# Kernel tuning notes

Measured on AMD Instinct MI355X. Metric: run time of the kernel, lower is better.

## Reference

```python
import jax, jax.numpy as jnp
import numpy as np

N, E, H, L, IN, OUT = 50000, 800000, 64, 14, 128, 112
MSG_EPS = 1e-7   # GENConv message epsilon
LN_EPS = 1e-5    # torch.nn.LayerNorm default eps


def setup_inputs() -> dict:
    key = jax.random.key(0)
    ks = jax.random.split(key, 8)
    s = 0.05
    x = jax.random.normal(ks[0], (N, IN), jnp.float32)
    edge_index = jax.random.randint(ks[1], (2, E), 0, N, dtype=jnp.int64)
    enc_W = jax.random.normal(ks[2], (IN, H), jnp.float32) * s
    enc_b = jnp.zeros((H,), jnp.float32)
    ln_g = jnp.ones((L, H), jnp.float32)
    ln_b = jnp.zeros((L, H), jnp.float32)
    mlp_W = jax.random.normal(ks[3], (L, H, H), jnp.float32) * s
    mlp_b = jnp.zeros((L, H), jnp.float32)
    pred_W = jax.random.normal(ks[4], (H, OUT), jnp.float32) * s
    pred_b = jnp.zeros((OUT,), jnp.float32)
    return dict(x=x, edge_index=edge_index, enc_W=enc_W, enc_b=enc_b,
                ln_g=ln_g, ln_b=ln_b, mlp_W=mlp_W, mlp_b=mlp_b,
                pred_W=pred_W, pred_b=pred_b)


def _layernorm(h, g, b):
    mu = jnp.mean(h, axis=-1, keepdims=True)
    var = jnp.mean(jnp.square(h - mu), axis=-1, keepdims=True)  # biased, as torch
    return (h - mu) * jax.lax.rsqrt(var + LN_EPS) * g + b


def _genconv(h, src, dst, W, b):
    # GENConv: msg = relu(x_src) + eps; softmax aggregation (t=1) over dst; out = Linear(x + agg)
    msg = jax.nn.relu(h[src]) + MSG_EPS                    # [E, H]
    mmax = jax.ops.segment_max(msg, dst, num_segments=N)   # [N, H]
    mmax = jnp.where(jnp.isfinite(mmax), mmax, 0.0)         # empty segments
    ex = jnp.exp(msg - mmax[dst])                           # [E, H]
    denom = jax.ops.segment_sum(ex, dst, num_segments=N)    # [N, H]
    num = jax.ops.segment_sum(msg * ex, dst, num_segments=N)
    agg = num / jnp.maximum(denom, 1e-16)                   # 0 for isolated nodes
    return (h + agg) @ W + b


def reference(x, edge_index, enc_W, enc_b, ln_g, ln_b, mlp_W, mlp_b, pred_W, pred_b):
    src, dst = edge_index[0], edge_index[1]
    h = x @ enc_W + enc_b                       # node feature encoder
    h = _genconv(h, src, dst, mlp_W[0], mlp_b[0])  # first GCN (no pre-norm in res+)

    def body(h, params):
        g, bl, W, b = params
        h2 = jax.nn.relu(_layernorm(h, g, bl))  # dropout is identity (eval)
        h = _genconv(h2, src, dst, W, b) + h    # residual
        return h, None

    h, _ = jax.lax.scan(body, h, (ln_g[:L - 1], ln_b[:L - 1], mlp_W[1:], mlp_b[1:]))
    return h @ pred_W + pred_b
```

## Files before the change

kernel.cpp:

```cpp
#include <hip/hip_runtime.h>
#include <hip/hip_bf16.h>

#define NN 50000
#define EE 800000
#define HD 64
#define LL 14
#define IND 128
#define OUTD 112
#define LN2 0.69314718056f

typedef __attribute__((ext_vector_type(8))) short short8;
typedef __attribute__((ext_vector_type(4))) float float4_;
typedef __attribute__((ext_vector_type(4))) unsigned short ushort4_;

__device__ __forceinline__ short bf16_hi(float x) {
    return (short)(__float_as_uint(x) >> 16);
}
__device__ __forceinline__ float bf16_f(short s) {
    return __uint_as_float(((unsigned)(unsigned short)s) << 16);
}
__device__ __forceinline__ unsigned short f2b_rne(float x) {
    unsigned u = __float_as_uint(x);
    u += 0x7fffu + ((u >> 16) & 1u);
    return (unsigned short)(u >> 16);
}

__device__ __forceinline__ void split8(const float* p, short8& hi, short8& lo) {
    float4_ a = *(const float4_*)p;
    float4_ b = *(const float4_*)(p + 4);
    float v[8] = {a[0], a[1], a[2], a[3], b[0], b[1], b[2], b[3]};
    #pragma unroll
    for (int j = 0; j < 8; ++j) {
        short h = bf16_hi(v[j]);
        hi[j] = h;
        lo[j] = bf16_hi(v[j] - bf16_f(h));
    }
}

__device__ __forceinline__ void load_b(const float* __restrict__ W, int ldw,
                                       int colbase, int krow, short8& hi, short8& lo) {
    #pragma unroll
    for (int j = 0; j < 8; ++j) {
        float wv = W[(krow + j) * ldw + colbase];
        short h = bf16_hi(wv);
        hi[j] = h;
        lo[j] = bf16_hi(wv - bf16_f(h));
    }
}

__device__ __forceinline__ float4_ mm3(short8 ah, short8 al, short8 bh, short8 bl,
                                       float4_ acc) {
    acc = __builtin_amdgcn_mfma_f32_16x16x32_bf16(ah, bh, acc, 0, 0, 0);
    acc = __builtin_amdgcn_mfma_f32_16x16x32_bf16(al, bh, acc, 0, 0, 0);
    acc = __builtin_amdgcn_mfma_f32_16x16x32_bf16(ah, bl, acc, 0, 0, 0);
    return acc;
}

#define ACCQ(q, sv, nv) { \
    float p0_ = __uint_as_float((q).x << 16); \
    float p1_ = __uint_as_float((q).x & 0xffff0000u); \
    float p2_ = __uint_as_float((q).y << 16); \
    float p3_ = __uint_as_float((q).y & 0xffff0000u); \
    sv[0] += p0_; sv[1] += p1_; sv[2] += p2_; sv[3] += p3_; \
    nv[0] = fmaf(p0_, __log2f(p0_), nv[0]); \
    nv[1] = fmaf(p1_, __log2f(p1_), nv[1]); \
    nv[2] = fmaf(p2_, __log2f(p2_), nv[2]); \
    nv[3] = fmaf(p3_, __log2f(p3_), nv[3]); }


__global__ void k_hist(const int* __restrict__ ei, int* __restrict__ cnt,
                       int* __restrict__ rank) {
    int e = blockIdx.x * blockDim.x + threadIdx.x;
    if (e < EE) rank[e] = atomicAdd(&cnt[ei[EE + e]], 1);
}

__global__ __launch_bounds__(1024) void k_scan1(const int* __restrict__ deg,
                                                int* __restrict__ excl,
                                                int* __restrict__ bsum) {
    __shared__ int ws[16];
    int tid = threadIdx.x, lane = tid & 63, w = tid >> 6;
    int gid = blockIdx.x * 1024 + tid;
    int v = (gid < NN) ? deg[gid] : 0;
    int x = v;
    #pragma unroll
    for (int d = 1; d < 64; d <<= 1) {
        int y = __shfl_up(x, d);
        if (lane >= d) x += y;
    }
    if (lane == 63) ws[w] = x;
    __syncthreads();
    if (tid == 0) {
        int acc = 0;
        for (int i = 0; i < 16; i++) { int t = ws[i]; ws[i] = acc; acc += t; }
        bsum[blockIdx.x] = acc;
    }
    __syncthreads();
    if (gid < NN) excl[gid] = x - v + ws[w];
}

__global__ void k_scan2(const int* __restrict__ bsum, int* __restrict__ boff, int nb) {
    int lane = threadIdx.x & 63;
    int v = (lane < nb) ? bsum[lane] : 0;
    int x = v;
    #pragma unroll
    for (int d = 1; d < 64; d <<= 1) {
        int y = __shfl_up(x, d);
        if (lane >= d) x += y;
    }
    if (lane < nb) boff[lane] = x - v;
}

__global__ __launch_bounds__(1024) void k_scan3(int* __restrict__ rp,
                                                const int* __restrict__ boff) {
    int gid = blockIdx.x * 1024 + threadIdx.x;
    if (gid < NN) rp[gid] += boff[blockIdx.x];
    if (gid == 0) rp[NN] = EE;
}

__global__ void k_scatter(const int* __restrict__ ei, const int* __restrict__ rp,
                          const int* __restrict__ rank, int* __restrict__ csrc) {
    int e = blockIdx.x * blockDim.x + threadIdx.x;
    if (e < EE) {
        int d = ei[EE + e];
        csrc[rp[d] + rank[e]] = ei[e];
    }
}


__global__ __launch_bounds__(256) void k_dhist(const int* __restrict__ deg,
                                               int* __restrict__ bhist) {
    __shared__ int lh[64];
    int tid = threadIdx.x;
    if (tid < 64) lh[tid] = 0;
    __syncthreads();
    int n = blockIdx.x * 256 + tid;
    if (n < NN) atomicAdd(&lh[63 - min(deg[n], 63)], 1);
    __syncthreads();
    if (tid < 64 && lh[tid]) atomicAdd(&bhist[tid], lh[tid]);
}

__global__ void k_dscan(const int* __restrict__ bhist, int* __restrict__ gboff) {
    int lane = threadIdx.x & 63;
    int v = bhist[lane];
    int x = v;
    #pragma unroll
    for (int d = 1; d < 64; d <<= 1) {
        int y = __shfl_up(x, d);
        if (lane >= d) x += y;
    }
    gboff[lane] = x - v;
}

__global__ __launch_bounds__(256) void k_dscatter(const int* __restrict__ deg,
                                                  const int* __restrict__ rp,
                                                  int* __restrict__ gboff,
                                                  int4* __restrict__ nd) {
    __shared__ int lh[64], lbase[64];
    int tid = threadIdx.x;
    if (tid < 64) lh[tid] = 0;
    __syncthreads();
    int n = blockIdx.x * 256 + tid;
    int b = 0, lr = 0;
    if (n < NN) {
        b = 63 - min(deg[n], 63);
        lr = atomicAdd(&lh[b], 1);
    }
    __syncthreads();
    if (tid < 64) lbase[tid] = lh[tid] ? atomicAdd(&gboff[tid], lh[tid]) : 0;
    __syncthreads();
    if (n < NN) {
        int pos = lbase[b] + lr;
        nd[pos] = make_int4(n, rp[n], rp[n + 1] - rp[n], 0);
    }
}


__global__ __launch_bounds__(256) void k_enc(const float* __restrict__ x,
                                             const float* __restrict__ W,
                                             const float* __restrict__ b,
                                             float* __restrict__ h,
                                             unsigned short* __restrict__ P0,
                                             unsigned short* __restrict__ P1) {
    __shared__ float X[16 * 132];
    int tid = threadIdx.x, lane = tid & 63, w = tid >> 6;
    int nb = blockIdx.x * 16;
    int nq = lane >> 4, nr = lane & 15;
    int colbase = w * 16 + nr;

    if (blockIdx.x == 0 && tid < HD) {
        P0[(size_t)NN * HD + tid] = 0x3f80;
        P1[(size_t)NN * HD + tid] = 0x3f80;
    }

    {
        const float* src = x + (size_t)nb * IND + tid * 8;
        float4_ a = *(const float4_*)src;
        float4_ c = *(const float4_*)(src + 4);
        int m = tid >> 4, k8 = 8 * (tid & 15);
        *(float4_*)&X[m * 132 + k8] = a;
        *(float4_*)&X[m * 132 + k8 + 4] = c;
    }
    __syncthreads();

    float4_ acc = {};
    #pragma unroll
    for (int t = 0; t < 4; ++t) {
        short8 ah, al, bh, bl;
        split8(&X[nr * 132 + t * 32 + nq * 8], ah, al);
        load_b(W, HD, colbase, t * 32 + nq * 8, bh, bl);
        acc = mm3(ah, al, bh, bl, acc);
    }

    float bias = b[colbase];
    #pragma unroll
    for (int r = 0; r < 4; ++r) {
        int node = nb + nq * 4 + r;
        float y = acc[r] + bias;
        h[node * HD + colbase] = y;
        float msg = fminf(fmaxf(y, 0.f) + 1e-7f, 50.f);
        P0[node * HD + colbase] = f2b_rne(__expf(msg));
    }
}

__device__ __forceinline__ void gtail(const unsigned* __restrict__ Pb,
                                      const int* __restrict__ csrc,
                                      int beg, int deg, int g, int co, int lane,
                                      float4_& sv, float4_& nv, int& waste) {
    for (int chunk = 64; chunk < deg; chunk += 64) {
        int my = (chunk + lane < deg) ? csrc[beg + chunk + lane] : NN;
        int cnt = min(64, deg - chunk);
        int nb4 = (cnt + 3) >> 2;
        waste += nb4 * 4 - cnt;
        for (int k = 0; k < nb4; ++k) {
            int e = __shfl(my, k * 4 + g);
            uint2 q = *(const uint2*)(Pb + (((unsigned)e) << 5) + co);
            ACCQ(q, sv, nv);
        }
    }
}

__device__ __forceinline__ void finish_node(float4_ sv, float4_ nv, int waste,
                                            int pnode, int row, int g, int ci,
                                            const float* __restrict__ selfh,
                                            uint2 selfq, float* __restrict__ T) {
    float t0 = sv[0], t1 = sv[1], t2 = sv[2], t3 = sv[3];
    float u0 = nv[0], u1 = nv[1], u2 = nv[2], u3 = nv[3];
    #pragma unroll
    for (int d = 16; d < 64; d <<= 1) {
        t0 += __shfl_xor(t0, d); t1 += __shfl_xor(t1, d);
        t2 += __shfl_xor(t2, d); t3 += __shfl_xor(t3, d);
        u0 += __shfl_xor(u0, d); u1 += __shfl_xor(u1, d);
        u2 += __shfl_xor(u2, d); u3 += __shfl_xor(u3, d);
    }
    if (g == 0) {
        float wf = (float)waste;
        float a0 = LN2 * u0 / fmaxf(t0 - wf, 1e-16f);
        float a1 = LN2 * u1 / fmaxf(t1 - wf, 1e-16f);
        float a2 = LN2 * u2 / fmaxf(t2 - wf, 1e-16f);
        float a3 = LN2 * u3 / fmaxf(t3 - wf, 1e-16f);
        float4_ xv;
        if (selfh) {
            float4_ sf = *(const float4_*)&selfh[(size_t)pnode * HD + ci * 4];
            xv[0] = sf[0] + a0; xv[1] = sf[1] + a1;
            xv[2] = sf[2] + a2; xv[3] = sf[3] + a3;
        } else {
            unsigned d0 = selfq.x, d1 = selfq.y;
            xv[0] = LN2 * __log2f(__uint_as_float(d0 << 16)) - 1e-7f + a0;
            xv[1] = LN2 * __log2f(__uint_as_float(d0 & 0xffff0000u)) - 1e-7f + a1;
            xv[2] = LN2 * __log2f(__uint_as_float(d1 << 16)) - 1e-7f + a2;
            xv[3] = LN2 * __log2f(__uint_as_float(d1 & 0xffff0000u)) - 1e-7f + a3;
        }
        *(float4_*)&T[row * 68 + ci * 4] = xv;
    }
}

__global__ __launch_bounds__(256, 4) void k_layer(const unsigned short* __restrict__ Pin,
                                                  const float* __restrict__ selfh,
                                                  const float* __restrict__ hres,
                                                  float* __restrict__ hout,
                                                  unsigned short* __restrict__ Pout,
                                                  const int4* __restrict__ nd,
                                                  const int* __restrict__ csrc,
                                                  const float* __restrict__ W,
                                                  const float* __restrict__ b,
                                                  const float* __restrict__ gnext,
                                                  const float* __restrict__ bnext) {
    __shared__ float T[16 * 68];
    __shared__ int PN[16];
    int tid = threadIdx.x, lane = tid & 63, w = tid >> 6;
    int nb = blockIdx.x * 16;
    int nq = lane >> 4, nr = lane & 15;
    int colbase = w * 16 + nr;

    if (tid < 16) PN[tid] = nd[nb + tid].x;

    short8 Bhi[2], Blo[2];
    #pragma unroll
    for (int t = 0; t < 2; ++t)
        load_b(W, HD, colbase, t * 32 + nq * 8, Bhi[t], Blo[t]);

    int g = lane >> 4;
    int ci = lane & 15;
    int co = ci << 1;
    const unsigned* Pb = (const unsigned*)Pin;

    int4 dsc0 = nd[nb + w * 4 + 0];
    int4 dsc1 = nd[nb + w * 4 + 1];
    int4 dsc2 = nd[nb + w * 4 + 2];
    int4 dsc3 = nd[nb + w * 4 + 3];
    int p0n = dsc0.x, r0 = dsc0.y, dA = dsc0.z;
    int p1n = dsc1.x, r1 = dsc1.y, dB = dsc1.z;
    int p2n = dsc2.x, r2 = dsc2.y, dC = dsc2.z;
    int p3n = dsc3.x, r3 = dsc3.y, dD = dsc3.z;

    int myA = (lane < dA) ? csrc[r0 + lane] : NN;
    int myB = (lane < dB) ? csrc[r1 + lane] : NN;
    int myC = (lane < dC) ? csrc[r2 + lane] : NN;
    int myD = (lane < dD) ? csrc[r3 + lane] : NN;

    uint2 sq0 = {0, 0}, sq1 = {0, 0}, sq2 = {0, 0}, sq3 = {0, 0};
    if (!selfh) {
        sq0 = *(const uint2*)(Pb + (((unsigned)p0n) << 5) + co);
        sq1 = *(const uint2*)(Pb + (((unsigned)p1n) << 5) + co);
        sq2 = *(const uint2*)(Pb + (((unsigned)p2n) << 5) + co);
        sq3 = *(const uint2*)(Pb + (((unsigned)p3n) << 5) + co);
    }

    int cA = min(dA, 64), cB = min(dB, 64), cC = min(dC, 64), cD = min(dD, 64);
    int nk = (max(max(cA, cB), max(cC, cD)) + 3) >> 2;
    int wA = nk * 4 - cA, wB = nk * 4 - cB, wC = nk * 4 - cC, wD = nk * 4 - cD;

    float4_ sA = {}, nA = {}, sB = {}, nB = {}, sC = {}, nC = {}, sD = {}, nD = {};

    #pragma unroll 2
    for (int k = 0; k < nk; ++k) {
        int sidx = k * 4 + g;
        int e0 = __shfl(myA, sidx);
        int e1 = __shfl(myB, sidx);
        int e2 = __shfl(myC, sidx);
        int e3 = __shfl(myD, sidx);
        uint2 q0 = *(const uint2*)(Pb + (((unsigned)e0) << 5) + co);
        uint2 q1 = *(const uint2*)(Pb + (((unsigned)e1) << 5) + co);
        uint2 q2 = *(const uint2*)(Pb + (((unsigned)e2) << 5) + co);
        uint2 q3 = *(const uint2*)(Pb + (((unsigned)e3) << 5) + co);
        ACCQ(q0, sA, nA);
        ACCQ(q1, sB, nB);
        ACCQ(q2, sC, nC);
        ACCQ(q3, sD, nD);
    }
    if (dA > 64) gtail(Pb, csrc, r0, dA, g, co, lane, sA, nA, wA);
    if (dB > 64) gtail(Pb, csrc, r1, dB, g, co, lane, sB, nB, wB);
    if (dC > 64) gtail(Pb, csrc, r2, dC, g, co, lane, sC, nC, wC);
    if (dD > 64) gtail(Pb, csrc, r3, dD, g, co, lane, sD, nD, wD);

    finish_node(sA, nA, wA, p0n, w * 4 + 0, g, ci, selfh, sq0, T);
    finish_node(sB, nB, wB, p1n, w * 4 + 1, g, ci, selfh, sq1, T);
    finish_node(sC, nC, wC, p2n, w * 4 + 2, g, ci, selfh, sq2, T);
    finish_node(sD, nD, wD, p3n, w * 4 + 3, g, ci, selfh, sq3, T);
    __syncthreads();

    short8 Ahi[2], Alo[2];
    #pragma unroll
    for (int t = 0; t < 2; ++t)
        split8(&T[nr * 68 + t * 32 + nq * 8], Ahi[t], Alo[t]);
    __syncthreads();

    float4_ acc = {};
    #pragma unroll
    for (int t = 0; t < 2; ++t)
        acc = mm3(Ahi[t], Alo[t], Bhi[t], Blo[t], acc);

    float bias = b[colbase];
    #pragma unroll
    for (int r = 0; r < 4; ++r) {
        int m = nq * 4 + r;
        int pn = PN[m];
        float v = acc[r] + bias;
        if (hres) v += hres[pn * HD + colbase];
        hout[pn * HD + colbase] = v;
        T[m * 68 + colbase] = v;
    }
    if (!Pout) return;
    __syncthreads();

    int m = tid >> 4, c4 = (tid & 15) * 4;
    float4_ vv = *(const float4_*)&T[m * 68 + c4];
    float ps_ = (vv[0] + vv[1]) + (vv[2] + vv[3]);
    float pq_ = (vv[0] * vv[0] + vv[1] * vv[1]) + (vv[2] * vv[2] + vv[3] * vv[3]);
    #pragma unroll
    for (int d = 8; d; d >>= 1) {
        ps_ += __shfl_xor(ps_, d);
        pq_ += __shfl_xor(pq_, d);
    }
    float mu = ps_ * (1.f / 64.f);
    float var = pq_ * (1.f / 64.f) - mu * mu;
    float inv = rsqrtf(fmaxf(var, 0.f) + 1e-5f);
    float4_ g4 = *(const float4_*)&gnext[c4];
    float4_ b4 = *(const float4_*)&bnext[c4];
    ushort4_ po;
    #pragma unroll
    for (int j = 0; j < 4; ++j) {
        float y = fmaxf((vv[j] - mu) * inv * g4[j] + b4[j], 0.f);
        float msg = fminf(y + 1e-7f, 50.f);
        po[j] = f2b_rne(__expf(msg));
    }
    *(ushort4_*)&Pout[(size_t)PN[m] * HD + c4] = po;
}


__global__ __launch_bounds__(256) void k_pred(const float* __restrict__ h,
                                              const float* __restrict__ W,
                                              const float* __restrict__ b,
                                              float* __restrict__ out) {
    __shared__ float T[16 * 68];
    int tid = threadIdx.x, lane = tid & 63, w = tid >> 6;
    int nb = blockIdx.x * 16;
    int nq = lane >> 4, nr = lane & 15;

    {
        const float* src = h + (size_t)nb * HD + tid * 4;
        float4_ a = *(const float4_*)src;
        int m = tid >> 4, k4 = 4 * (tid & 15);
        *(float4_*)&T[m * 68 + k4] = a;
    }
    __syncthreads();

    short8 Ahi[2], Alo[2];
    #pragma unroll
    for (int t = 0; t < 2; ++t)
        split8(&T[nr * 68 + t * 32 + nq * 8], Ahi[t], Alo[t]);

    for (int tt = w; tt < 7; tt += 4) {
        int colbase = tt * 16 + nr;
        float4_ acc = {};
        #pragma unroll
        for (int t = 0; t < 2; ++t) {
            short8 bh, bl;
            load_b(W, OUTD, colbase, t * 32 + nq * 8, bh, bl);
            acc = mm3(Ahi[t], Alo[t], bh, bl, acc);
        }
        float bias = b[colbase];
        #pragma unroll
        for (int r = 0; r < 4; ++r) {
            int node = nb + nq * 4 + r;
            out[node * OUTD + colbase] = acc[r] + bias;
        }
    }
}


extern "C" void kernel_launch(void* const* d_in, const int* in_sizes, int n_in,
                              void* d_out, int out_size, void* d_ws, size_t ws_size,
                              hipStream_t stream) {
    const float* x    = (const float*)d_in[0];
    const int*   ei   = (const int*)d_in[1];
    const float* encW = (const float*)d_in[2];
    const float* encb = (const float*)d_in[3];
    const float* lng  = (const float*)d_in[4];
    const float* lnb  = (const float*)d_in[5];
    const float* mlpW = (const float*)d_in[6];
    const float* mlpb = (const float*)d_in[7];
    const float* pW   = (const float*)d_in[8];
    const float* pb   = (const float*)d_in[9];
    float* out = (float*)d_out;

    int4* nd = (int4*)d_ws;
    float* hA  = (float*)(nd + NN);
    float* hB  = hA + (size_t)NN * HD;
    unsigned short* PA = (unsigned short*)(hB + (size_t)NN * HD);
    unsigned short* PB = PA + (size_t)(NN + 1) * HD;
    int* rp    = (int*)(PB + (size_t)(NN + 1) * HD);
    int* cnt   = rp + (NN + 1);
    int* csrc  = cnt + NN;
    int* rank  = csrc + EE;
    int* bsum  = rank + EE;
    int* boff  = bsum + 64;
    int* bhist = boff + 64;
    int* gboff = bhist + 64;

    hipMemsetAsync(cnt, 0, NN * sizeof(int), stream);
    hipMemsetAsync(bhist, 0, 64 * sizeof(int), stream);
    k_hist<<<(EE + 255) / 256, 256, 0, stream>>>(ei, cnt, rank);
    const int NB = (NN + 1023) / 1024;
    k_scan1<<<NB, 1024, 0, stream>>>(cnt, rp, bsum);
    k_scan2<<<1, 64, 0, stream>>>(bsum, boff, NB);
    k_scan3<<<NB, 1024, 0, stream>>>(rp, boff);
    k_scatter<<<(EE + 255) / 256, 256, 0, stream>>>(ei, rp, rank, csrc);

    const int NDB = (NN + 255) / 256;
    k_dhist<<<NDB, 256, 0, stream>>>(cnt, bhist);
    k_dscan<<<1, 64, 0, stream>>>(bhist, gboff);
    k_dscatter<<<NDB, 256, 0, stream>>>(cnt, rp, gboff, nd);

    k_enc<<<NN / 16, 256, 0, stream>>>(x, encW, encb, hA, PA, PB);

    k_layer<<<NN / 16, 256, 0, stream>>>(PA, hA, nullptr, hB, PB, nd, csrc,
                                         mlpW, mlpb, lng, lnb);

    float* hres = hB;
    float* hdst = hA;
    unsigned short* pc = PB;
    unsigned short* pn = PA;
    for (int l = 1; l < LL; ++l) {
        bool last = (l == LL - 1);
        k_layer<<<NN / 16, 256, 0, stream>>>(pc, nullptr, hres, hdst,
                                             last ? nullptr : pn,
                                             nd, csrc,
                                             mlpW + (size_t)l * HD * HD,
                                             mlpb + (size_t)l * HD,
                                             last ? nullptr : lng + (size_t)l * HD,
                                             last ? nullptr : lnb + (size_t)l * HD);
        float* t = hres; hres = hdst; hdst = t;
        unsigned short* u = pc; pc = pn; pn = u;
    }

    k_pred<<<NN / 16, 256, 0, stream>>>(hres, pW, pb, out);
}
```

Before: 646.8 us.

## Gather 8 bf16 features per lane with 16-byte loads, processing nodes in pairs

The neighbor gather in the layer kernel now has each lane load a uint4 (8 bf16 values) instead of a uint2 (4 values). Eight edges are processed per wave step instead of four, and the cross-lane reduction gets one extra shuffle stage. The four destination nodes per wave are handled as two sequential pairs, which limits the growth in accumulator registers. The wider loads are meant to cut gather instruction count and raise bytes per request, but per-node padding waste grows with the 8-edge granularity, and only two rows are gathered concurrently instead of four, which lowers memory-level parallelism.

```diff
diff --git a/kernel.cpp b/kernel.cpp
--- a/kernel.cpp
+++ b/kernel.cpp
@@ -56,16 +56,25 @@
     return acc;
 }
 
-#define ACCQ(q, sv, nv) { \
+#define ACCQ8(q, sv, nv) { \
     float p0_ = __uint_as_float((q).x << 16); \
     float p1_ = __uint_as_float((q).x & 0xffff0000u); \
     float p2_ = __uint_as_float((q).y << 16); \
     float p3_ = __uint_as_float((q).y & 0xffff0000u); \
+    float p4_ = __uint_as_float((q).z << 16); \
+    float p5_ = __uint_as_float((q).z & 0xffff0000u); \
+    float p6_ = __uint_as_float((q).w << 16); \
+    float p7_ = __uint_as_float((q).w & 0xffff0000u); \
     sv[0] += p0_; sv[1] += p1_; sv[2] += p2_; sv[3] += p3_; \
+    sv[4] += p4_; sv[5] += p5_; sv[6] += p6_; sv[7] += p7_; \
     nv[0] = fmaf(p0_, __log2f(p0_), nv[0]); \
     nv[1] = fmaf(p1_, __log2f(p1_), nv[1]); \
     nv[2] = fmaf(p2_, __log2f(p2_), nv[2]); \
-    nv[3] = fmaf(p3_, __log2f(p3_), nv[3]); }
+    nv[3] = fmaf(p3_, __log2f(p3_), nv[3]); \
+    nv[4] = fmaf(p4_, __log2f(p4_), nv[4]); \
+    nv[5] = fmaf(p5_, __log2f(p5_), nv[5]); \
+    nv[6] = fmaf(p6_, __log2f(p6_), nv[6]); \
+    nv[7] = fmaf(p7_, __log2f(p7_), nv[7]); }
 
 
 __global__ void k_hist(const int* __restrict__ ei, int* __restrict__ cnt,
@@ -222,55 +231,54 @@
     }
 }
 
-__device__ __forceinline__ void gtail(const unsigned* __restrict__ Pb,
-                                      const int* __restrict__ csrc,
-                                      int beg, int deg, int g, int co, int lane,
-                                      float4_& sv, float4_& nv, int& waste) {
+__device__ __forceinline__ void gtail8(const unsigned* __restrict__ Pb,
+                                       const int* __restrict__ csrc,
+                                       int beg, int deg, int og, int co4, int lane,
+                                       float* s, float* n, int& waste) {
     for (int chunk = 64; chunk < deg; chunk += 64) {
+        int cnt = min(64, deg - chunk);
         int my = (chunk + lane < deg) ? csrc[beg + chunk + lane] : NN;
-        int cnt = min(64, deg - chunk);
-        int nb4 = (cnt + 3) >> 2;
-        waste += nb4 * 4 - cnt;
-        for (int k = 0; k < nb4; ++k) {
-            int e = __shfl(my, k * 4 + g);
-            uint2 q = *(const uint2*)(Pb + (((unsigned)e) << 5) + co);
-            ACCQ(q, sv, nv);
-        }
-    }
-}
-
-__device__ __forceinline__ void finish_node(float4_ sv, float4_ nv, int waste,
-                                            int pnode, int row, int g, int ci,
-                                            const float* __restrict__ selfh,
-                                            uint2 selfq, float* __restrict__ T) {
-    float t0 = sv[0], t1 = sv[1], t2 = sv[2], t3 = sv[3];
-    float u0 = nv[0], u1 = nv[1], u2 = nv[2], u3 = nv[3];
-    #pragma unroll
-    for (int d = 16; d < 64; d <<= 1) {
-        t0 += __shfl_xor(t0, d); t1 += __shfl_xor(t1, d);
-        t2 += __shfl_xor(t2, d); t3 += __shfl_xor(t3, d);
-        u0 += __shfl_xor(u0, d); u1 += __shfl_xor(u1, d);
-        u2 += __shfl_xor(u2, d); u3 += __shfl_xor(u3, d);
-    }
-    if (g == 0) {
+        int nr8 = (cnt + 7) >> 3;
+        waste += nr8 * 8 - cnt;
+        for (int k = 0; k < nr8; ++k) {
+            int e = __shfl(my, k * 8 + og);
+            uint4 q = *(const uint4*)(Pb + (((unsigned)e) << 5) + co4);
+            ACCQ8(q, s, n);
+        }
+    }
+}
+
+__device__ __forceinline__ void finish8(float* s, float* n, int waste, int pnode,
+                                        int row, int og, int ci8,
+                                        const float* __restrict__ selfh,
+                                        uint4 selfq, float* __restrict__ T) {
+    #pragma unroll
+    for (int j = 0; j < 8; ++j) { s[j] += __shfl_xor(s[j], 8);  n[j] += __shfl_xor(n[j], 8); }
+    #pragma unroll
+    for (int j = 0; j < 8; ++j) { s[j] += __shfl_xor(s[j], 16); n[j] += __shfl_xor(n[j], 16); }
+    #pragma unroll
+    for (int j = 0; j < 8; ++j) { s[j] += __shfl_xor(s[j], 32); n[j] += __shfl_xor(n[j], 32); }
+    if (og == 0) {
         float wf = (float)waste;
-        float a0 = LN2 * u0 / fmaxf(t0 - wf, 1e-16f);
-        float a1 = LN2 * u1 / fmaxf(t1 - wf, 1e-16f);
-        float a2 = LN2 * u2 / fmaxf(t2 - wf, 1e-16f);
-        float a3 = LN2 * u3 / fmaxf(t3 - wf, 1e-16f);
-        float4_ xv;
-        if (selfh) {
-            float4_ sf = *(const float4_*)&selfh[(size_t)pnode * HD + ci * 4];
-            xv[0] = sf[0] + a0; xv[1] = sf[1] + a1;
-            xv[2] = sf[2] + a2; xv[3] = sf[3] + a3;
-        } else {
-            unsigned d0 = selfq.x, d1 = selfq.y;
-            xv[0] = LN2 * __log2f(__uint_as_float(d0 << 16)) - 1e-7f + a0;
-            xv[1] = LN2 * __log2f(__uint_as_float(d0 & 0xffff0000u)) - 1e-7f + a1;
-            xv[2] = LN2 * __log2f(__uint_as_float(d1 << 16)) - 1e-7f + a2;
-            xv[3] = LN2 * __log2f(__uint_as_float(d1 & 0xffff0000u)) - 1e-7f + a3;
-        }
-        *(float4_*)&T[row * 68 + ci * 4] = xv;
+        unsigned qq[4] = {selfq.x, selfq.y, selfq.z, selfq.w};
+        float xv[8];
+        #pragma unroll
+        for (int j = 0; j < 8; ++j) {
+            float a = LN2 * n[j] / fmaxf(s[j] - wf, 1e-16f);
+            float self;
+            if (selfh) {
+                self = selfh[(size_t)pnode * HD + ci8 * 8 + j];
+            } else {
+                unsigned word = qq[j >> 1];
+                unsigned bits = (j & 1) ? (word & 0xffff0000u) : (word << 16);
+                self = LN2 * __log2f(__uint_as_float(bits)) - 1e-7f;
+            }
+            xv[j] = self + a;
+        }
+        float4_ v0 = {xv[0], xv[1], xv[2], xv[3]};
+        float4_ v1 = {xv[4], xv[5], xv[6], xv[7]};
+        *(float4_*)&T[row * 68 + ci8 * 8] = v0;
+        *(float4_*)&T[row * 68 + ci8 * 8 + 4] = v1;
     }
 }
 
@@ -299,9 +307,9 @@
     for (int t = 0; t < 2; ++t)
         load_b(W, HD, colbase, t * 32 + nq * 8, Bhi[t], Blo[t]);
 
-    int g = lane >> 4;
-    int ci = lane & 15;
-    int co = ci << 1;
+    int og = lane >> 3;
+    int ci8 = lane & 7;
+    int co4 = ci8 * 4;
     const unsigned* Pb = (const unsigned*)Pin;
 
     int4 dsc0 = nd[nb + w * 4 + 0];
@@ -318,45 +326,60 @@
     int myC = (lane < dC) ? csrc[r2 + lane] : NN;
     int myD = (lane < dD) ? csrc[r3 + lane] : NN;
 
-    uint2 sq0 = {0, 0}, sq1 = {0, 0}, sq2 = {0, 0}, sq3 = {0, 0};
-    if (!selfh) {
-        sq0 = *(const uint2*)(Pb + (((unsigned)p0n) << 5) + co);
-        sq1 = *(const uint2*)(Pb + (((unsigned)p1n) << 5) + co);
-        sq2 = *(const uint2*)(Pb + (((unsigned)p2n) << 5) + co);
-        sq3 = *(const uint2*)(Pb + (((unsigned)p3n) << 5) + co);
-    }
-
     int cA = min(dA, 64), cB = min(dB, 64), cC = min(dC, 64), cD = min(dD, 64);
-    int nk = (max(max(cA, cB), max(cC, cD)) + 3) >> 2;
-    int wA = nk * 4 - cA, wB = nk * 4 - cB, wC = nk * 4 - cC, wD = nk * 4 - cD;
-
-    float4_ sA = {}, nA = {}, sB = {}, nB = {}, sC = {}, nC = {}, sD = {}, nD = {};
-
-    #pragma unroll 2
-    for (int k = 0; k < nk; ++k) {
-        int sidx = k * 4 + g;
-        int e0 = __shfl(myA, sidx);
-        int e1 = __shfl(myB, sidx);
-        int e2 = __shfl(myC, sidx);
-        int e3 = __shfl(myD, sidx);
-        uint2 q0 = *(const uint2*)(Pb + (((unsigned)e0) << 5) + co);
-        uint2 q1 = *(const uint2*)(Pb + (((unsigned)e1) << 5) + co);
-        uint2 q2 = *(const uint2*)(Pb + (((unsigned)e2) << 5) + co);
-        uint2 q3 = *(const uint2*)(Pb + (((unsigned)e3) << 5) + co);
-        ACCQ(q0, sA, nA);
-        ACCQ(q1, sB, nB);
-        ACCQ(q2, sC, nC);
-        ACCQ(q3, sD, nD);
-    }
-    if (dA > 64) gtail(Pb, csrc, r0, dA, g, co, lane, sA, nA, wA);
-    if (dB > 64) gtail(Pb, csrc, r1, dB, g, co, lane, sB, nB, wB);
-    if (dC > 64) gtail(Pb, csrc, r2, dC, g, co, lane, sC, nC, wC);
-    if (dD > 64) gtail(Pb, csrc, r3, dD, g, co, lane, sD, nD, wD);
-
-    finish_node(sA, nA, wA, p0n, w * 4 + 0, g, ci, selfh, sq0, T);
-    finish_node(sB, nB, wB, p1n, w * 4 + 1, g, ci, selfh, sq1, T);
-    finish_node(sC, nC, wC, p2n, w * 4 + 2, g, ci, selfh, sq2, T);
-    finish_node(sD, nD, wD, p3n, w * 4 + 3, g, ci, selfh, sq3, T);
+
+    float s0[8], n0[8], s1[8], n1[8];
+
+    {
+        uint4 sqA = {0, 0, 0, 0}, sqB = {0, 0, 0, 0};
+        if (!selfh) {
+            sqA = *(const uint4*)(Pb + (((unsigned)p0n) << 5) + co4);
+            sqB = *(const uint4*)(Pb + (((unsigned)p1n) << 5) + co4);
+        }
+        #pragma unroll
+        for (int j = 0; j < 8; ++j) { s0[j] = 0.f; n0[j] = 0.f; s1[j] = 0.f; n1[j] = 0.f; }
+        int nk = (max(cA, cB) + 7) >> 3;
+        int wA = nk * 8 - cA, wB = nk * 8 - cB;
+        #pragma unroll 2
+        for (int k = 0; k < nk; ++k) {
+            int sidx = k * 8 + og;
+            int eA = __shfl(myA, sidx);
+            int eB = __shfl(myB, sidx);
+            uint4 qA = *(const uint4*)(Pb + (((unsigned)eA) << 5) + co4);
+            uint4 qB = *(const uint4*)(Pb + (((unsigned)eB) << 5) + co4);
+            ACCQ8(qA, s0, n0);
+            ACCQ8(qB, s1, n1);
+        }
+        if (dA > 64) gtail8(Pb, csrc, r0, dA, og, co4, lane, s0, n0, wA);
+        if (dB > 64) gtail8(Pb, csrc, r1, dB, og, co4, lane, s1, n1, wB);
+        finish8(s0, n0, wA, p0n, w * 4 + 0, og, ci8, selfh, sqA, T);
+        finish8(s1, n1, wB, p1n, w * 4 + 1, og, ci8, selfh, sqB, T);
+    }
+    {
+        uint4 sqC = {0, 0, 0, 0}, sqD = {0, 0, 0, 0};
+        if (!selfh) {
+            sqC = *(const uint4*)(Pb + (((unsigned)p2n) << 5) + co4);
+            sqD = *(const uint4*)(Pb + (((unsigned)p3n) << 5) + co4);
+        }
+        #pragma unroll
+        for (int j = 0; j < 8; ++j) { s0[j] = 0.f; n0[j] = 0.f; s1[j] = 0.f; n1[j] = 0.f; }
+        int nk = (max(cC, cD) + 7) >> 3;
+        int wC = nk * 8 - cC, wD = nk * 8 - cD;
+        #pragma unroll 2
+        for (int k = 0; k < nk; ++k) {
+            int sidx = k * 8 + og;
+            int eC = __shfl(myC, sidx);
+            int eD = __shfl(myD, sidx);
+            uint4 qC = *(const uint4*)(Pb + (((unsigned)eC) << 5) + co4);
+            uint4 qD = *(const uint4*)(Pb + (((unsigned)eD) << 5) + co4);
+            ACCQ8(qC, s0, n0);
+            ACCQ8(qD, s1, n1);
+        }
+        if (dC > 64) gtail8(Pb, csrc, r2, dC, og, co4, lane, s0, n0, wC);
+        if (dD > 64) gtail8(Pb, csrc, r3, dD, og, co4, lane, s1, n1, wD);
+        finish8(s0, n0, wC, p2n, w * 4 + 2, og, ci8, selfh, sqC, T);
+        finish8(s1, n1, wD, p3n, w * 4 + 3, og, ci8, selfh, sqD, T);
+    }
     __syncthreads();
 
     short8 Ahi[2], Alo[2];
```

Measured after the change: 855.0 us. 32.2% more time.
